# Performance work log

Measured on AMD Instinct MI355X. Metric: run time of the kernel, lower is better.

## Reference

```python
import jax, jax.numpy as jnp
import numpy as np
import math

B, S, H = 4, 1024, 1024
NH, DH = 16, 64  # MULTI_HEAD, HIDDEN_SIZE_HEAD


def setup_inputs() -> dict:
    key = jax.random.key(0)
    ks = jax.random.split(key, 14)
    w = lambda k: (jax.random.normal(k, (H, H), dtype=jnp.float32) * 0.02)
    b = lambda k: (jax.random.normal(k, (H,), dtype=jnp.float32) * 0.02)
    return {
        "v": jax.random.normal(ks[0], (B, S, H), dtype=jnp.float32),
        "k": jax.random.normal(ks[1], (B, S, H), dtype=jnp.float32),
        "q": jax.random.normal(ks[2], (B, S, H), dtype=jnp.float32),
        "mask": jax.random.randint(ks[3], (B, 1, 1, S), 0, 2) == 1,
        "group_prob": jax.random.uniform(ks[4], (B, S, S), dtype=jnp.float32),
        "Wq": w(ks[5]), "bq": b(ks[6]),
        "Wk": w(ks[7]), "bk": b(ks[8]),
        "Wv": w(ks[9]), "bv": b(ks[10]),
        "Wm": w(ks[11]), "bm": b(ks[12]),
    }


def reference(v, k, q, mask, group_prob, Wq, bq, Wk, bk, Wv, bv, Wm, bm):
    nb = q.shape[0]
    inv_sqrt_dk = 1.0 / math.sqrt(DH)

    def proj(x, W, b):
        # torch Linear: x @ W.T + b, then split heads -> [B, NH, S, DH]
        y = jnp.einsum('bsh,oh->bso', x, W) + b
        return y.reshape(nb, -1, NH, DH).transpose(0, 2, 1, 3)

    qh = proj(q, Wq, bq)
    kh = proj(k, Wk, bk)
    vh = proj(v, Wv, bv)

    scores = jnp.einsum('bhqd,bhkd->bhqk', qh, kh) * inv_sqrt_dk
    scores = jnp.where(mask, jnp.float32(-1e9), scores)
    att = jax.nn.softmax(scores, axis=-1)
    # post-softmax group-prior scaling (the non-standard part)
    att = att * group_prob[:, None, :, :]
    # dropout in eval mode = identity
    out = jnp.einsum('bhqk,bhkd->bhqd', att, vh)
    out = out.transpose(0, 2, 1, 3).reshape(nb, -1, H)
    return jnp.einsum('bsh,oh->bso', out, Wm) + bm
```

## Files before the change

kernel.cpp:

```cpp
#include <hip/hip_runtime.h>

#define S_LEN 1024
#define NHEAD 16
#define DHEAD 64

typedef _Float16 half8 __attribute__((ext_vector_type(8)));
typedef _Float16 half4v __attribute__((ext_vector_type(4)));
typedef _Float16 half2v __attribute__((ext_vector_type(2)));
typedef float floatx4 __attribute__((ext_vector_type(4)));

#define QSCALE 0.125f
#define EXPSHIFT 4.0f
#define MASKBIAS -30000.0f

__device__ __forceinline__ void gll16(const _Float16* g, _Float16* s) {
    __builtin_amdgcn_global_load_lds(
        (const __attribute__((address_space(1))) void*)g,
        (__attribute__((address_space(3))) void*)s, 16, 0, 0);
}

struct SplitArgs {
    const float* src[8];
    _Float16* hi[8];
    int nblk[8];
    const int* mask;
    float* mbias;
};

__global__ __launch_bounds__(256) void split_all_kernel(SplitArgs a)
{
    int blk = blockIdx.x;
    if (blk < 4) {
        const int i = blk * 1024 + threadIdx.x * 4;
        int4 m = *(const int4*)&a.mask[i];
        float4 o;
        o.x = m.x ? MASKBIAS : 0.0f;
        o.y = m.y ? MASKBIAS : 0.0f;
        o.z = m.z ? MASKBIAS : 0.0f;
        o.w = m.w ? MASKBIAS : 0.0f;
        *(float4*)&a.mbias[i] = o;
        return;
    }
    blk -= 4;
    int seg = 0, off = 0;
    while (blk >= off + a.nblk[seg]) { off += a.nblk[seg]; ++seg; }
    const int base = (blk - off) * 4096 + threadIdx.x * 4;
#pragma unroll
    for (int u = 0; u < 4; ++u) {
        const int i = base + u * 1024;
        float4 v = *(const float4*)&a.src[seg][i];
        half4v h;
        h.x = (_Float16)v.x; h.y = (_Float16)v.y;
        h.z = (_Float16)v.z; h.w = (_Float16)v.w;
        *(half4v*)&a.hi[seg][i] = h;
    }
}

struct ProjArgs {
    const _Float16* A[3];
    const _Float16* B[3];
    const float* bias[3];
    _Float16* C[3];
};

__global__ __launch_bounds__(256, 3) void proj_gemm_kernel(ProjArgs p)
{
    __shared__ __align__(16) _Float16 Ab[128 * 64];
    __shared__ __align__(16) _Float16 Bb[128 * 64];

    const int bid = blockIdx.x;
    const int xcd = bid & 7;
    const int slot = bid >> 3;
    const int mg = slot & 3;
    const int bx = (slot >> 2) & 7;
    const int z  = slot >> 5;
    const int by = xcd + mg * 8;

    const _Float16* A = p.A[z];
    const _Float16* B = p.B[z];
    const float* bias = p.bias[z];
    _Float16* C = p.C[z];

    const int t = threadIdx.x;
    const int w = t >> 6;
    const int l = t & 63;
    const int r = l & 15;
    const int quad = l >> 4;
    const int k7 = r & 7;
    const int rr = l >> 3, ii = l & 7;
    const int wm = (w >> 1) * 64, wn = (w & 1) * 64;
    const int m0 = by * 128;
    const int n0 = bx * 128;

    floatx4 acc[4][4];
#pragma unroll
    for (int i = 0; i < 4; ++i)
#pragma unroll
        for (int j = 0; j < 4; ++j) acc[i][j] = (floatx4){0.f, 0.f, 0.f, 0.f};

    const _Float16* ssrc = (w < 2) ? A : B;
    _Float16* sdst = (w < 2) ? Ab : Bb;
    const int srow0 = (w < 2) ? m0 : n0;
    const int w01 = w & 1;

    auto stage = [&](int kt) {
        const int k0 = kt * 64;
#pragma unroll
        for (int c = 0; c < 8; ++c) {
            const int R = w01 * 64 + c * 8 + rr;
            const int j = ii ^ (R & 7);
            gll16(ssrc + (size_t)(srow0 + R) * 1024 + k0 + j * 8,
                  sdst + R * 64 + ii * 8);
        }
    };

    stage(0);
    for (int kt = 0; kt < 16; ++kt) {
        __syncthreads();

        half8 ah[4][2], bh[4][2];
#pragma unroll
        for (int i = 0; i < 4; ++i) {
            const int R = wm + i * 16 + r;
            ah[i][0] = *(const half8*)&Ab[R * 64 + ((quad ^ k7) << 3)];
            ah[i][1] = *(const half8*)&Ab[R * 64 + (((4 | quad) ^ k7) << 3)];
        }
#pragma unroll
        for (int j = 0; j < 4; ++j) {
            const int R = wn + j * 16 + r;
            bh[j][0] = *(const half8*)&Bb[R * 64 + ((quad ^ k7) << 3)];
            bh[j][1] = *(const half8*)&Bb[R * 64 + (((4 | quad) ^ k7) << 3)];
        }
        __syncthreads();

        if (kt + 1 < 16) stage(kt + 1);

#pragma unroll
        for (int c = 0; c < 2; ++c)
#pragma unroll
            for (int i = 0; i < 4; ++i)
#pragma unroll
                for (int j = 0; j < 4; ++j)
                    acc[i][j] = __builtin_amdgcn_mfma_f32_16x16x32_f16(
                        ah[i][c], bh[j][c], acc[i][j], 0, 0, 0);
    }

#pragma unroll
    for (int i = 0; i < 4; ++i)
#pragma unroll
        for (int j = 0; j < 4; ++j) {
            const int n = n0 + wn + j * 16 + r;
            const float bv = bias[n];
#pragma unroll
            for (int reg = 0; reg < 4; ++reg) {
                const int m = m0 + wm + i * 16 + quad * 4 + reg;
                float val = acc[i][j][reg] + bv;
                if (z == 0) val *= QSCALE;
                const int b = m >> 10, s = m & 1023;
                const int h = n >> 6, d = n & 63;
                const size_t idx = (z == 2)
                    ? (((size_t)(b * NHEAD + h)) * DHEAD + d) * S_LEN + s
                    : (((size_t)(b * NHEAD + h)) * S_LEN + s) * DHEAD + d;
                C[idx] = (_Float16)val;
            }
        }
}

__global__ __launch_bounds__(256, 2) void out_gemm_kernel(
    const _Float16* __restrict__ A, const _Float16* __restrict__ B,
    const float* __restrict__ bias, float* __restrict__ C)
{
    __shared__ __align__(16) _Float16 Ab[128 * 64];
    __shared__ __align__(16) _Float16 Bb[64 * 64];

    const int bid = blockIdx.x;
    const int xcd = bid & 7;
    const int slot = bid >> 3;
    const int by = xcd + (slot & 3) * 8;
    const int bx = slot >> 2;

    const int t = threadIdx.x;
    const int w = t >> 6;
    const int l = t & 63;
    const int r = l & 15;
    const int quad = l >> 4;
    const int k7 = r & 7;
    const int rr = l >> 3, ii = l & 7;
    const int m0 = by * 128, n0 = bx * 64;

    floatx4 acc[2][4];
#pragma unroll
    for (int mt = 0; mt < 2; ++mt)
#pragma unroll
        for (int j = 0; j < 4; ++j) acc[mt][j] = (floatx4){0.f, 0.f, 0.f, 0.f};

    auto stage = [&](int kt) {
        const int k0 = kt * 64;
        if (w < 2) {
#pragma unroll
            for (int c = 0; c < 8; ++c) {
                const int R = (w & 1) * 64 + c * 8 + rr;
                const int j = ii ^ (R & 7);
                gll16(A + (size_t)(m0 + R) * 1024 + k0 + j * 8,
                      Ab + R * 64 + ii * 8);
            }
        } else {
#pragma unroll
            for (int c = 0; c < 4; ++c) {
                const int R = (w - 2) * 32 + c * 8 + rr;
                const int j = ii ^ (R & 7);
                gll16(B + (size_t)(n0 + R) * 1024 + k0 + j * 8,
                      Bb + R * 64 + ii * 8);
            }
        }
    };

    stage(0);
    for (int kt = 0; kt < 16; ++kt) {
        __syncthreads();

        half8 ah[2][2], bh[4][2];
#pragma unroll
        for (int mt = 0; mt < 2; ++mt) {
            const int R = w * 32 + mt * 16 + r;
            ah[mt][0] = *(const half8*)&Ab[R * 64 + ((quad ^ k7) << 3)];
            ah[mt][1] = *(const half8*)&Ab[R * 64 + (((4 | quad) ^ k7) << 3)];
        }
#pragma unroll
        for (int j = 0; j < 4; ++j) {
            const int R = j * 16 + r;
            bh[j][0] = *(const half8*)&Bb[R * 64 + ((quad ^ k7) << 3)];
            bh[j][1] = *(const half8*)&Bb[R * 64 + (((4 | quad) ^ k7) << 3)];
        }
        __syncthreads();

        if (kt + 1 < 16) stage(kt + 1);

#pragma unroll
        for (int c = 0; c < 2; ++c)
#pragma unroll
            for (int mt = 0; mt < 2; ++mt)
#pragma unroll
                for (int j = 0; j < 4; ++j)
                    acc[mt][j] = __builtin_amdgcn_mfma_f32_16x16x32_f16(
                        ah[mt][c], bh[j][c], acc[mt][j], 0, 0, 0);
    }

#pragma unroll
    for (int mt = 0; mt < 2; ++mt)
#pragma unroll
        for (int j = 0; j < 4; ++j) {
            const int n = n0 + j * 16 + r;
            const float bv = bias[n];
#pragma unroll
            for (int reg = 0; reg < 4; ++reg) {
                const int m = m0 + w * 32 + mt * 16 + quad * 4 + reg;
                C[(size_t)m * 1024 + n] = acc[mt][j][reg] + bv;
            }
        }
}

__global__ __launch_bounds__(256, 2) void attention_mfma_kernel(
    const _Float16* __restrict__ Qhi, const _Float16* __restrict__ Khi,
    const _Float16* __restrict__ Vthi, const _Float16* __restrict__ gp16,
    const float* __restrict__ mbias, _Float16* __restrict__ OutHi)
{
    __shared__ __align__(16) _Float16 KhS[2][4096];
    __shared__ __align__(16) _Float16 VhS[2][4096];
    __shared__ __align__(16) _Float16 gpS[2][4096];
    __shared__ __align__(16) _Float16 PS[4096];
    __shared__ __align__(16) float mbS[1024];

    const int t = threadIdx.x;
    const int w = t >> 6;
    const int l = t & 63;
    const int lr = l & 15;
    const int quad = l >> 4;
    const int rr = l >> 3;
    const int ii = l & 7;

    const int Lid = ((blockIdx.x & 7) << 7) | (blockIdx.x >> 3);
    const int h   = Lid & 15;
    const int qt2 = (Lid >> 4) & 15;
    const int b   = Lid >> 8;
    const int q0  = qt2 * 64;
    const size_t hb = (size_t)(b * NHEAD + h) * (S_LEN * DHEAD);
    const int qg = q0 + w * 16 + lr;

    half8 qfh[2];
#pragma unroll
    for (int c = 0; c < 2; ++c) {
        const size_t off = hb + (size_t)qg * 64 + c * 32 + quad * 8;
        qfh[c] = *(const half8*)&Qhi[off];
    }

    float lpart = 0.0f;
    floatx4 Oa[4];
#pragma unroll
    for (int dt = 0; dt < 4; ++dt) Oa[dt] = (floatx4){0.f, 0.f, 0.f, 0.f};

    auto stageK = [&](int kt, int bf) {
        const int k0n = kt * 64;
#pragma unroll
        for (int c2 = 0; c2 < 2; ++c2) {
            const int c = w * 2 + c2;
            const int row = c * 8 + rr;
            const int j = ii ^ (row & 7);
            gll16(Khi + hb + (size_t)(k0n + row) * 64 + j * 8,
                  &KhS[bf][0] + c * 512 + l * 8);
        }
    };
    auto stageV = [&](int kt, int bf) {
        const int k0n = kt * 64;
#pragma unroll
        for (int c2 = 0; c2 < 2; ++c2) {
            const int i = w * 2 + c2;
            const int row = i * 8 + rr;
            const int j = ii ^ (row & 7);
            gll16(Vthi + hb + (size_t)row * S_LEN + k0n + j * 8,
                  &VhS[bf][0] + i * 512 + l * 8);
        }
    };
    auto stageGP = [&](int kt, int bf) {
        const int k0n = kt * 64;
#pragma unroll
        for (int c = 0; c < 2; ++c) {
            const int s = c * 256 + t;
            const int row = s >> 3;
            const int chl = (s & 7) ^ (row & 7);
            gll16(gp16 + ((size_t)(b * S_LEN + q0 + row)) * S_LEN + k0n + chl * 8,
                  &gpS[bf][0] + s * 8);
        }
    };

    stageK(0, 0);
    stageV(0, 0);
    stageGP(0, 0);
    *(float4*)&mbS[t * 4] = *(const float4*)&mbias[b * S_LEN + t * 4];
    __syncthreads();

    const int qloc = w * 16 + lr;
    const int q7 = qloc & 7;

    for (int kt = 0; kt < 16; ++kt) {
        const int bf = kt & 1;
        const int k0 = kt * 64;

        if (kt + 1 < 16) {
            stageK(kt + 1, bf ^ 1);
            stageV(kt + 1, bf ^ 1);
            stageGP(kt + 1, bf ^ 1);
        }

        floatx4 sc[4];
#pragma unroll
        for (int j = 0; j < 4; ++j) {
            const int key = j * 16 + lr;
            const int base = key * 64;
            const int k7a = key & 7;
            const half8 kh0 = *(const half8*)&KhS[bf][base + (quad ^ k7a) * 8];
            const half8 kh1 = *(const half8*)&KhS[bf][base + ((4 + quad) ^ k7a) * 8];
            floatx4 a = *(const floatx4*)&mbS[k0 + j * 16 + quad * 4];
            a = __builtin_amdgcn_mfma_f32_16x16x32_f16(kh0, qfh[0], a, 0, 0, 0);
            a = __builtin_amdgcn_mfma_f32_16x16x32_f16(kh1, qfh[1], a, 0, 0, 0);
            sc[j] = a;
        }

#pragma unroll
        for (int j = 0; j < 4; ++j) {
            const int ch = j * 2 + (quad >> 1);
            const half4v g4 = *(const half4v*)&gpS[bf][qloc * 64 +
                ((ch ^ q7) << 3) + (quad & 1) * 4];
            const float p0 = __expf(sc[j][0] - EXPSHIFT);
            const float p1 = __expf(sc[j][1] - EXPSHIFT);
            const float p2 = __expf(sc[j][2] - EXPSHIFT);
            const float p3 = __expf(sc[j][3] - EXPSHIFT);
            lpart += (p0 + p1) + (p2 + p3);
            half2v a01 = {(_Float16)p0, (_Float16)p1};
            half2v a23 = {(_Float16)p2, (_Float16)p3};
            const half2v g01 = {g4.x, g4.y};
            const half2v g23 = {g4.z, g4.w};
            a01 *= g01;
            a23 *= g23;
            half4v res;
            res.x = a01.x; res.y = a01.y; res.z = a23.x; res.w = a23.y;
            *(half4v*)&PS[qloc * 64 + ((ch ^ q7) << 3) + (quad & 1) * 4] = res;
        }

        half8 pf[2];
        pf[0] = *(const half8*)&PS[qloc * 64 + ((quad ^ q7) << 3)];
        pf[1] = *(const half8*)&PS[qloc * 64 + (((4 + quad) ^ q7) << 3)];
#pragma unroll
        for (int dt = 0; dt < 4; ++dt) {
            const int d = dt * 16 + lr;
            const int base = d * 64, d7 = d & 7;
            const half8 vh0 = *(const half8*)&VhS[bf][base + (quad ^ d7) * 8];
            const half8 vh1 = *(const half8*)&VhS[bf][base + ((4 + quad) ^ d7) * 8];
            floatx4 a = Oa[dt];
            a = __builtin_amdgcn_mfma_f32_16x16x32_f16(pf[0], vh0, a, 0, 0, 0);
            a = __builtin_amdgcn_mfma_f32_16x16x32_f16(pf[1], vh1, a, 0, 0, 0);
            Oa[dt] = a;
        }

        __syncthreads();
    }

    lpart += __shfl_xor(lpart, 16, 64);
    lpart += __shfl_xor(lpart, 32, 64);

#pragma unroll
    for (int rg = 0; rg < 4; ++rg) {
        const float li = 1.0f / __shfl(lpart, quad * 4 + rg, 64);
        const int s = q0 + w * 16 + quad * 4 + rg;
#pragma unroll
        for (int dt = 0; dt < 4; ++dt) {
            const float val = Oa[dt][rg] * li;
            const size_t idx = ((size_t)(b * S_LEN + s)) * 1024 + h * 64 + dt * 16 + lr;
            OutHi[idx] = (_Float16)val;
        }
    }
}

extern "C" void kernel_launch(void* const* d_in, const int* in_sizes, int n_in,
                              void* d_out, int out_size, void* d_ws, size_t ws_size,
                              hipStream_t stream) {
    const float* v    = (const float*)d_in[0];
    const float* k    = (const float*)d_in[1];
    const float* q    = (const float*)d_in[2];
    const int*   mask = (const int*)d_in[3];
    const float* gp   = (const float*)d_in[4];
    const float* Wq   = (const float*)d_in[5];
    const float* bq   = (const float*)d_in[6];
    const float* Wk   = (const float*)d_in[7];
    const float* bk   = (const float*)d_in[8];
    const float* Wv   = (const float*)d_in[9];
    const float* bv   = (const float*)d_in[10];
    const float* Wm   = (const float*)d_in[11];
    const float* bm   = (const float*)d_in[12];
    float* out = (float*)d_out;

    uint8_t* w8 = (uint8_t*)d_ws;
    const size_t MB = 1024 * 1024;
    _Float16* q_h  = (_Float16*)(w8 + 0 * MB);
    _Float16* k_h  = (_Float16*)(w8 + 8 * MB);
    _Float16* v_h  = (_Float16*)(w8 + 16 * MB);
    _Float16* Wq_h = (_Float16*)(w8 + 24 * MB);
    _Float16* Wk_h = (_Float16*)(w8 + 26 * MB);
    _Float16* Wv_h = (_Float16*)(w8 + 28 * MB);
    _Float16* Wm_h = (_Float16*)(w8 + 30 * MB);
    _Float16* Qh   = (_Float16*)(w8 + 32 * MB);
    _Float16* Kh   = (_Float16*)(w8 + 40 * MB);
    _Float16* Vt   = (_Float16*)(w8 + 48 * MB);
    _Float16* gp16 = (_Float16*)(w8 + 56 * MB);
    _Float16* at   = (_Float16*)(w8 + 0 * MB);
    float* mb_f = (ws_size >= 64 * MB + 16384)
                ? (float*)(w8 + 64 * MB) : (float*)d_out;

    SplitArgs sa;
    sa.src[0] = q;  sa.hi[0] = q_h;  sa.nblk[0] = 1024;
    sa.src[1] = k;  sa.hi[1] = k_h;  sa.nblk[1] = 1024;
    sa.src[2] = v;  sa.hi[2] = v_h;  sa.nblk[2] = 1024;
    sa.src[3] = Wq; sa.hi[3] = Wq_h; sa.nblk[3] = 256;
    sa.src[4] = Wk; sa.hi[4] = Wk_h; sa.nblk[4] = 256;
    sa.src[5] = Wv; sa.hi[5] = Wv_h; sa.nblk[5] = 256;
    sa.src[6] = Wm; sa.hi[6] = Wm_h; sa.nblk[6] = 256;
    sa.src[7] = gp; sa.hi[7] = gp16; sa.nblk[7] = 1024;
    sa.mask = mask;
    sa.mbias = mb_f;
    split_all_kernel<<<5124, 256, 0, stream>>>(sa);

    ProjArgs pa;
    pa.A[0] = q_h; pa.B[0] = Wq_h; pa.bias[0] = bq; pa.C[0] = Qh;
    pa.A[1] = k_h; pa.B[1] = Wk_h; pa.bias[1] = bk; pa.C[1] = Kh;
    pa.A[2] = v_h; pa.B[2] = Wv_h; pa.bias[2] = bv; pa.C[2] = Vt;
    proj_gemm_kernel<<<768, 256, 0, stream>>>(pa);

    attention_mfma_kernel<<<1024, 256, 0, stream>>>(
        Qh, Kh, Vt, gp16, mb_f, at);

    out_gemm_kernel<<<512, 256, 0, stream>>>(
        at, Wm_h, bm, out);
}
```

Before: 240.8 us.

## Pre-permute group_prob tiles into MFMA fragment order and load directly to registers

The split kernel now converts group_prob to fp16 in 64x64 tiles and writes each tile permuted so that each attention thread's fragment is 16 contiguous halfs. The attention kernel then loads those fragments straight into registers, double-buffered across iterations, instead of staging them through LDS. This drops the gp shared buffer, so launch bounds go from 2 to 3 blocks per CU. The cost is an LDS transpose step in the split kernel and more registers per thread, which may spill under the tighter occupancy bound.

```diff
diff --git a/kernel.cpp b/kernel.cpp
--- a/kernel.cpp
+++ b/kernel.cpp
@@ -20,15 +20,18 @@
 }
 
 struct SplitArgs {
-    const float* src[8];
-    _Float16* hi[8];
-    int nblk[8];
+    const float* src[7];
+    _Float16* hi[7];
+    int nblk[7];
     const int* mask;
     float* mbias;
+    const float* gp;
+    _Float16* gpt;
 };
 
 __global__ __launch_bounds__(256) void split_all_kernel(SplitArgs a)
 {
+    __shared__ _Float16 G[64 * 64];
     int blk = blockIdx.x;
     if (blk < 4) {
         const int i = blk * 1024 + threadIdx.x * 4;
@@ -41,6 +44,32 @@
         *(float4*)&a.mbias[i] = o;
         return;
     }
+    if (blk >= 4 + 4096) {
+        const int g = blk - (4 + 4096);
+        const int b = g >> 8, qt2 = (g >> 4) & 15, kt = g & 15;
+        const float* src = a.gp + ((size_t)(b * S_LEN + qt2 * 64)) * S_LEN + kt * 64;
+        const int t = threadIdx.x;
+#pragma unroll
+        for (int it = 0; it < 4; ++it) {
+            const int s = it * 256 + t;
+            const int row = s >> 4, cl = s & 15;
+            float4 v = *(const float4*)&src[(size_t)row * S_LEN + cl * 4];
+            half4v hh;
+            hh.x = (_Float16)v.x; hh.y = (_Float16)v.y;
+            hh.z = (_Float16)v.z; hh.w = (_Float16)v.w;
+            *(half4v*)&G[row * 64 + ((cl ^ (row & 15)) << 2)] = hh;
+        }
+        __syncthreads();
+        const int w = t >> 6, lr = t & 15, quad = (t >> 4) & 3;
+        const int qloc = w * 16 + lr;
+        _Float16* dst = a.gpt + (size_t)g * 4096 + t * 16;
+#pragma unroll
+        for (int j = 0; j < 4; ++j) {
+            const int c = (j * 4 + quad) ^ (qloc & 15);
+            *(half4v*)&dst[j * 4] = *(const half4v*)&G[qloc * 64 + (c << 2)];
+        }
+        return;
+    }
     blk -= 4;
     int seg = 0, off = 0;
     while (blk >= off + a.nblk[seg]) { off += a.nblk[seg]; ++seg; }
@@ -260,14 +289,13 @@
         }
 }
 
-__global__ __launch_bounds__(256, 2) void attention_mfma_kernel(
+__global__ __launch_bounds__(256, 3) void attention_mfma_kernel(
     const _Float16* __restrict__ Qhi, const _Float16* __restrict__ Khi,
-    const _Float16* __restrict__ Vthi, const _Float16* __restrict__ gp16,
+    const _Float16* __restrict__ Vthi, const _Float16* __restrict__ gpt,
     const float* __restrict__ mbias, _Float16* __restrict__ OutHi)
 {
     __shared__ __align__(16) _Float16 KhS[2][4096];
     __shared__ __align__(16) _Float16 VhS[2][4096];
-    __shared__ __align__(16) _Float16 gpS[2][4096];
     __shared__ __align__(16) _Float16 PS[4096];
     __shared__ __align__(16) float mbS[1024];
 
@@ -286,6 +314,7 @@
     const int q0  = qt2 * 64;
     const size_t hb = (size_t)(b * NHEAD + h) * (S_LEN * DHEAD);
     const int qg = q0 + w * 16 + lr;
+    const _Float16* gbase = gpt + ((size_t)((b * 16 + qt2) * 16)) * 4096;
 
     half8 qfh[2];
 #pragma unroll
@@ -321,21 +350,15 @@
                   &VhS[bf][0] + i * 512 + l * 8);
         }
     };
-    auto stageGP = [&](int kt, int bf) {
-        const int k0n = kt * 64;
-#pragma unroll
-        for (int c = 0; c < 2; ++c) {
-            const int s = c * 256 + t;
-            const int row = s >> 3;
-            const int chl = (s & 7) ^ (row & 7);
-            gll16(gp16 + ((size_t)(b * S_LEN + q0 + row)) * S_LEN + k0n + chl * 8,
-                  &gpS[bf][0] + s * 8);
-        }
+    auto loadG = [&](half8 (&g)[2], int kt) {
+        g[0] = *(const half8*)&gbase[(size_t)kt * 4096 + t * 16];
+        g[1] = *(const half8*)&gbase[(size_t)kt * 4096 + t * 16 + 8];
     };
 
+    half8 gc[2], gn[2];
     stageK(0, 0);
     stageV(0, 0);
-    stageGP(0, 0);
+    loadG(gc, 0);
     *(float4*)&mbS[t * 4] = *(const float4*)&mbias[b * S_LEN + t * 4];
     __syncthreads();
 
@@ -349,7 +372,7 @@
         if (kt + 1 < 16) {
             stageK(kt + 1, bf ^ 1);
             stageV(kt + 1, bf ^ 1);
-            stageGP(kt + 1, bf ^ 1);
+            loadG(gn, kt + 1);
         }
 
         floatx4 sc[4];
@@ -368,9 +391,7 @@
 
 #pragma unroll
         for (int j = 0; j < 4; ++j) {
-            const int ch = j * 2 + (quad >> 1);
-            const half4v g4 = *(const half4v*)&gpS[bf][qloc * 64 +
-                ((ch ^ q7) << 3) + (quad & 1) * 4];
+            const int hi = j >> 1, gof = (j & 1) * 4;
             const float p0 = __expf(sc[j][0] - EXPSHIFT);
             const float p1 = __expf(sc[j][1] - EXPSHIFT);
             const float p2 = __expf(sc[j][2] - EXPSHIFT);
@@ -378,12 +399,13 @@
             lpart += (p0 + p1) + (p2 + p3);
             half2v a01 = {(_Float16)p0, (_Float16)p1};
             half2v a23 = {(_Float16)p2, (_Float16)p3};
-            const half2v g01 = {g4.x, g4.y};
-            const half2v g23 = {g4.z, g4.w};
+            const half2v g01 = {gc[hi][gof + 0], gc[hi][gof + 1]};
+            const half2v g23 = {gc[hi][gof + 2], gc[hi][gof + 3]};
             a01 *= g01;
             a23 *= g23;
             half4v res;
             res.x = a01.x; res.y = a01.y; res.z = a23.x; res.w = a23.y;
+            const int ch = j * 2 + (quad >> 1);
             *(half4v*)&PS[qloc * 64 + ((ch ^ q7) << 3) + (quad & 1) * 4] = res;
         }
 
@@ -403,6 +425,11 @@
         }
 
         __syncthreads();
+
+        if (kt + 1 < 16) {
+            gc[0] = gn[0];
+            gc[1] = gn[1];
+        }
     }
 
     lpart += __shfl_xor(lpart, 16, 64);
@@ -451,7 +478,7 @@
     _Float16* Qh   = (_Float16*)(w8 + 32 * MB);
     _Float16* Kh   = (_Float16*)(w8 + 40 * MB);
     _Float16* Vt   = (_Float16*)(w8 + 48 * MB);
-    _Float16* gp16 = (_Float16*)(w8 + 56 * MB);
+    _Float16* gpt  = (_Float16*)(w8 + 56 * MB);
     _Float16* at   = (_Float16*)(w8 + 0 * MB);
     float* mb_f = (ws_size >= 64 * MB + 16384)
                 ? (float*)(w8 + 64 * MB) : (float*)d_out;
@@ -464,9 +491,10 @@
     sa.src[4] = Wk; sa.hi[4] = Wk_h; sa.nblk[4] = 256;
     sa.src[5] = Wv; sa.hi[5] = Wv_h; sa.nblk[5] = 256;
     sa.src[6] = Wm; sa.hi[6] = Wm_h; sa.nblk[6] = 256;
-    sa.src[7] = gp; sa.hi[7] = gp16; sa.nblk[7] = 1024;
     sa.mask = mask;
     sa.mbias = mb_f;
+    sa.gp = gp;
+    sa.gpt = gpt;
     split_all_kernel<<<5124, 256, 0, stream>>>(sa);
 
     ProjArgs pa;
@@ -476,7 +504,7 @@
     proj_gemm_kernel<<<768, 256, 0, stream>>>(pa);
 
     attention_mfma_kernel<<<1024, 256, 0, stream>>>(
-        Qh, Kh, Vt, gp16, mb_f, at);
+        Qh, Kh, Vt, gpt, mb_f, at);
 
     out_gemm_kernel<<<512, 256, 0, stream>>>(
         at, Wm_h, bm, out);
```

Result: no change. 236.7 us (-1.7%).
